# Kernel optimization log

Hardware: AMD Instinct MI355X
Metric: run time of the kernel (lower is better)

## Reference

```python
import jax, jax.numpy as jnp
import numpy as np

B, K, D = 8192, 256, 128


def setup_inputs() -> dict:
    key = jax.random.key(0)
    k1, k2 = jax.random.split(key)
    z = jax.random.normal(k1, (B, D), dtype=jnp.float32)
    centroids = jax.random.normal(k2, (K, D), dtype=jnp.float32)
    logvar = jnp.zeros((K, D), dtype=jnp.float32)
    return {"z": z, "centroids": centroids, "logvar": logvar}


def reference(z, centroids, logvar):
    # Mahalanobis (diagonal-covariance) distance of each z row to each centroid.
    # dist[b,k] = sum_d (z[b,d] - mu[k,d])^2 / var[k,d]
    diff = z[:, None, :] - centroids[None, :, :]          # (B, K, D)
    var = jnp.exp(logvar)[None, :, :]                      # (1, K, D)
    dist = jnp.sum(diff * diff / var, axis=2)              # (B, K)
    # Soft assignments: softmax over clusters of -0.5 * dist (stable softmax).
    return jax.nn.softmax(-0.5 * dist, axis=1)             # (B, K)
```

## Files before the change

### kernel.cpp

```cpp
#include <hip/hip_runtime.h>
#include <hip/hip_bf16.h>


typedef short     bf16x8  __attribute__((ext_vector_type(8)));
typedef float     f32x4   __attribute__((ext_vector_type(4)));
typedef unsigned short ushort_t;

constexpr int Bn = 8192, Kn = 256, Dn = 128;

constexpr size_t BH_OFF = 0;
constexpr size_t BL_OFF = (size_t)16 * 8 * 64 * 8;
constexpr size_t CV_OFF = 2 * BL_OFF;
constexpr size_t NEED_BYTES = CV_OFF * 2 + (size_t)Kn * 4;

__device__ __forceinline__ short bfbits(__hip_bfloat16 h) {
    return __builtin_bit_cast(short, h);
}

__device__ __forceinline__ void split8(const float* f, bf16x8& hi, bf16x8& lo) {
    #pragma unroll
    for (int p = 0; p < 4; ++p) {
        const float2 fp = make_float2(f[2 * p], f[2 * p + 1]);
        const __hip_bfloat162 h2 = __float22bfloat162_rn(fp);
        hi[2 * p]     = bfbits(h2.x);
        hi[2 * p + 1] = bfbits(h2.y);
        const float2 rp = make_float2(fp.x - __bfloat162float(h2.x),
                                      fp.y - __bfloat162float(h2.y));
        const __hip_bfloat162 l2 = __float22bfloat162_rn(rp);
        lo[2 * p]     = bfbits(l2.x);
        lo[2 * p + 1] = bfbits(l2.y);
    }
}

__global__ __launch_bounds__(512)
void prep(const float* __restrict__ cent, const float* __restrict__ lvar,
          ushort_t* __restrict__ ws)
{
    __shared__ float red2[16][8];
    const int tid = threadIdx.x;
    const int kk  = tid >> 6;
    const int l   = tid & 63;
    const int lg  = l >> 4;
    const int ll  = l & 15;
    const int cg  = blockIdx.x;
    const int col = cg * 16 + ll;
    const int d0  = kk * 16 + lg * 4;

    const float4 cv = *reinterpret_cast<const float4*>(cent + (size_t)col * Dn + d0);
    const float4 l4 = *reinterpret_cast<const float4*>(lvar + (size_t)col * Dn + d0);
    const float a0 = __expf(-l4.x), a1 = __expf(-l4.y);
    const float a2 = __expf(-l4.z), a3 = __expf(-l4.w);
    const float f[8] = {a0, -2.0f * cv.x * a0, a1, -2.0f * cv.y * a1,
                        a2, -2.0f * cv.z * a2, a3, -2.0f * cv.w * a3};
    bf16x8 hi, lo;
    split8(f, hi, lo);
    const size_t off = ((size_t)(cg * 8 + kk) * 64 + l) * 8;
    *reinterpret_cast<bf16x8*>(ws + BH_OFF + off) = hi;
    *reinterpret_cast<bf16x8*>(ws + BL_OFF + off) = lo;

    float cp = cv.x * cv.x * a0 + cv.y * cv.y * a1 +
               cv.z * cv.z * a2 + cv.w * cv.w * a3;
    cp += __shfl_xor(cp, 16);
    cp += __shfl_xor(cp, 32);
    if (lg == 0) red2[ll][kk] = cp;
    __syncthreads();
    if (tid < 16) {
        float s = 0.f;
        #pragma unroll
        for (int q = 0; q < 8; ++q) s += red2[tid][q];
        reinterpret_cast<float*>(ws + CV_OFF)[cg * 16 + tid] = s;
    }
}

__global__ __launch_bounds__(1024, 4)
void gmm_main(const float* __restrict__ z, const ushort_t* __restrict__ ws,
              float* __restrict__ out)
{
    __shared__ ushort_t Ah[2 * 8 * 64 * 8];
    __shared__ ushort_t Al[2 * 8 * 64 * 8];
    __shared__ float red[32][16];

    const int tid = threadIdx.x;
    const int w   = tid >> 6;
    const int l   = tid & 63;
    const int lg  = l >> 4;
    const int ll  = l & 15;
    const int b0  = blockIdx.x * 32;
    const int n0  = w * 16;

    {
        const int r   = tid >> 9;
        const int kks = (tid >> 6) & 7;
        const int row = r * 16 + ll;
        const int d0  = kks * 16 + lg * 4;
        const float4 v = *reinterpret_cast<const float4*>(
            z + (size_t)(b0 + row) * Dn + d0);
        const float f[8] = {v.x * v.x, v.x, v.y * v.y, v.y,
                            v.z * v.z, v.z, v.w * v.w, v.w};
        bf16x8 hi, lo;
        split8(f, hi, lo);
        const int off = tid * 8;
        *reinterpret_cast<bf16x8*>(&Ah[off]) = hi;
        *reinterpret_cast<bf16x8*>(&Al[off]) = lo;
    }
    __syncthreads();

    const ushort_t* BH = ws + BH_OFF;
    const ushort_t* BL = ws + BL_OFF;
    const float*  cvec = reinterpret_cast<const float*>(ws + CV_OFF);

    f32x4 acc0 = (f32x4){0.f, 0.f, 0.f, 0.f};
    f32x4 acc1 = (f32x4){0.f, 0.f, 0.f, 0.f};

    const size_t bbase = (size_t)w * 4096 + (size_t)l * 8;

    bf16x8 bh = *reinterpret_cast<const bf16x8*>(BH + bbase);
    bf16x8 bl = *reinterpret_cast<const bf16x8*>(BL + bbase);

    #pragma unroll
    for (int kk = 0; kk < 8; ++kk) {
        bf16x8 nbh, nbl;
        if (kk < 7) {
            nbh = *reinterpret_cast<const bf16x8*>(BH + bbase + (kk + 1) * 512);
            nbl = *reinterpret_cast<const bf16x8*>(BL + bbase + (kk + 1) * 512);
        }
        const int ao = kk * 512 + l * 8;
        const bf16x8 a0h = *reinterpret_cast<const bf16x8*>(&Ah[ao]);
        const bf16x8 a0l = *reinterpret_cast<const bf16x8*>(&Al[ao]);
        const bf16x8 a1h = *reinterpret_cast<const bf16x8*>(&Ah[4096 + ao]);
        const bf16x8 a1l = *reinterpret_cast<const bf16x8*>(&Al[4096 + ao]);

        acc0 = __builtin_amdgcn_mfma_f32_16x16x32_bf16(a0h, bh, acc0, 0, 0, 0);
        acc1 = __builtin_amdgcn_mfma_f32_16x16x32_bf16(a1h, bh, acc1, 0, 0, 0);
        acc0 = __builtin_amdgcn_mfma_f32_16x16x32_bf16(a0h, bl, acc0, 0, 0, 0);
        acc1 = __builtin_amdgcn_mfma_f32_16x16x32_bf16(a1h, bl, acc1, 0, 0, 0);
        acc0 = __builtin_amdgcn_mfma_f32_16x16x32_bf16(a0l, bh, acc0, 0, 0, 0);
        acc1 = __builtin_amdgcn_mfma_f32_16x16x32_bf16(a1l, bh, acc1, 0, 0, 0);

        bh = nbh; bl = nbl;
    }

    const float ck = cvec[n0 + ll];

    float dv[2][4];
    #pragma unroll
    for (int r = 0; r < 4; ++r) { dv[0][r] = acc0[r] + ck; dv[1][r] = acc1[r] + ck; }

    #pragma unroll
    for (int mi = 0; mi < 2; ++mi)
        #pragma unroll
        for (int r = 0; r < 4; ++r) {
            float t = dv[mi][r];
            t = fminf(t, __shfl_xor(t, 1));
            t = fminf(t, __shfl_xor(t, 2));
            t = fminf(t, __shfl_xor(t, 4));
            t = fminf(t, __shfl_xor(t, 8));
            if (ll == 0) red[mi * 16 + lg * 4 + r][w] = t;
        }
    __syncthreads();

    float gm[2][4];
    #pragma unroll
    for (int mi = 0; mi < 2; ++mi)
        #pragma unroll
        for (int r = 0; r < 4; ++r) {
            const int row = mi * 16 + lg * 4 + r;
            const f32x4* rp = reinterpret_cast<const f32x4*>(&red[row][0]);
            f32x4 m4 = rp[0];
            #pragma unroll
            for (int q = 1; q < 4; ++q) {
                f32x4 v = rp[q];
                m4[0] = fminf(m4[0], v[0]); m4[1] = fminf(m4[1], v[1]);
                m4[2] = fminf(m4[2], v[2]); m4[3] = fminf(m4[3], v[3]);
            }
            gm[mi][r] = fminf(fminf(m4[0], m4[1]), fminf(m4[2], m4[3]));
        }
    __syncthreads();

    float pv[2][4];
    #pragma unroll
    for (int mi = 0; mi < 2; ++mi)
        #pragma unroll
        for (int r = 0; r < 4; ++r) {
            const float p = __expf(-0.5f * (dv[mi][r] - gm[mi][r]));
            pv[mi][r] = p;
            float s = p;
            s += __shfl_xor(s, 1);
            s += __shfl_xor(s, 2);
            s += __shfl_xor(s, 4);
            s += __shfl_xor(s, 8);
            if (ll == 0) red[mi * 16 + lg * 4 + r][w] = s;
        }
    __syncthreads();

    #pragma unroll
    for (int mi = 0; mi < 2; ++mi)
        #pragma unroll
        for (int r = 0; r < 4; ++r) {
            const int row = mi * 16 + lg * 4 + r;
            const f32x4* rp = reinterpret_cast<const f32x4*>(&red[row][0]);
            f32x4 s4 = rp[0];
            #pragma unroll
            for (int q = 1; q < 4; ++q) {
                f32x4 v = rp[q];
                s4[0] += v[0]; s4[1] += v[1]; s4[2] += v[2]; s4[3] += v[3];
            }
            const float inv = 1.0f / ((s4[0] + s4[1]) + (s4[2] + s4[3]));
            out[(size_t)(b0 + row) * Kn + n0 + ll] = pv[mi][r] * inv;
        }
}

__global__ __launch_bounds__(1024, 4)
void gmm_fused(const float* __restrict__ z, const float* __restrict__ cent,
               const float* __restrict__ lvar, float* __restrict__ out)
{
    __shared__ ushort_t Ah[2 * 8 * 64 * 8];
    __shared__ ushort_t Al[2 * 8 * 64 * 8];
    __shared__ float red[32][16];

    const int tid = threadIdx.x;
    const int w   = tid >> 6;
    const int l   = tid & 63;
    const int lg  = l >> 4;
    const int ll  = l & 15;
    const int b0  = blockIdx.x * 32;
    const int n0  = w * 16;

    {
        const int r   = tid >> 9;
        const int kks = (tid >> 6) & 7;
        const int row = r * 16 + ll;
        const int d0  = kks * 16 + lg * 4;
        const float4 v = *reinterpret_cast<const float4*>(
            z + (size_t)(b0 + row) * Dn + d0);
        const float f[8] = {v.x * v.x, v.x, v.y * v.y, v.y,
                            v.z * v.z, v.z, v.w * v.w, v.w};
        bf16x8 hi, lo;
        split8(f, hi, lo);
        const int off = tid * 8;
        *reinterpret_cast<bf16x8*>(&Ah[off]) = hi;
        *reinterpret_cast<bf16x8*>(&Al[off]) = lo;
    }
    __syncthreads();

    f32x4 acc0 = (f32x4){0.f, 0.f, 0.f, 0.f};
    f32x4 acc1 = (f32x4){0.f, 0.f, 0.f, 0.f};
    float cpart = 0.0f;
    const size_t crow = (size_t)(n0 + ll) * Dn + lg * 4;

    float4 cv = *reinterpret_cast<const float4*>(cent + crow);
    float4 v4 = *reinterpret_cast<const float4*>(lvar + crow);

    #pragma unroll
    for (int kk = 0; kk < 8; ++kk) {
        float4 ncv, nv4;
        if (kk < 7) {
            ncv = *reinterpret_cast<const float4*>(cent + crow + (kk + 1) * 16);
            nv4 = *reinterpret_cast<const float4*>(lvar + crow + (kk + 1) * 16);
        }
        const float a0 = __expf(-v4.x), a1 = __expf(-v4.y);
        const float a2 = __expf(-v4.z), a3 = __expf(-v4.w);
        const float f[8] = {a0, -2.0f * cv.x * a0, a1, -2.0f * cv.y * a1,
                            a2, -2.0f * cv.z * a2, a3, -2.0f * cv.w * a3};
        bf16x8 Bh, Bl;
        split8(f, Bh, Bl);
        cpart += cv.x * cv.x * a0 + cv.y * cv.y * a1 +
                 cv.z * cv.z * a2 + cv.w * cv.w * a3;

        const int ao = kk * 512 + l * 8;
        const bf16x8 a0h = *reinterpret_cast<const bf16x8*>(&Ah[ao]);
        const bf16x8 a0l = *reinterpret_cast<const bf16x8*>(&Al[ao]);
        const bf16x8 a1h = *reinterpret_cast<const bf16x8*>(&Ah[4096 + ao]);
        const bf16x8 a1l = *reinterpret_cast<const bf16x8*>(&Al[4096 + ao]);

        acc0 = __builtin_amdgcn_mfma_f32_16x16x32_bf16(a0h, Bh, acc0, 0, 0, 0);
        acc1 = __builtin_amdgcn_mfma_f32_16x16x32_bf16(a1h, Bh, acc1, 0, 0, 0);
        acc0 = __builtin_amdgcn_mfma_f32_16x16x32_bf16(a0h, Bl, acc0, 0, 0, 0);
        acc1 = __builtin_amdgcn_mfma_f32_16x16x32_bf16(a1h, Bl, acc1, 0, 0, 0);
        acc0 = __builtin_amdgcn_mfma_f32_16x16x32_bf16(a0l, Bh, acc0, 0, 0, 0);
        acc1 = __builtin_amdgcn_mfma_f32_16x16x32_bf16(a1l, Bh, acc1, 0, 0, 0);

        cv = ncv; v4 = nv4;
    }
    cpart += __shfl_xor(cpart, 16);
    cpart += __shfl_xor(cpart, 32);
    const float ck = cpart;

    float dv[2][4];
    #pragma unroll
    for (int r = 0; r < 4; ++r) { dv[0][r] = acc0[r] + ck; dv[1][r] = acc1[r] + ck; }

    #pragma unroll
    for (int mi = 0; mi < 2; ++mi)
        #pragma unroll
        for (int r = 0; r < 4; ++r) {
            float t = dv[mi][r];
            t = fminf(t, __shfl_xor(t, 1));
            t = fminf(t, __shfl_xor(t, 2));
            t = fminf(t, __shfl_xor(t, 4));
            t = fminf(t, __shfl_xor(t, 8));
            if (ll == 0) red[mi * 16 + lg * 4 + r][w] = t;
        }
    __syncthreads();

    float gm[2][4];
    #pragma unroll
    for (int mi = 0; mi < 2; ++mi)
        #pragma unroll
        for (int r = 0; r < 4; ++r) {
            const int row = mi * 16 + lg * 4 + r;
            const f32x4* rp = reinterpret_cast<const f32x4*>(&red[row][0]);
            f32x4 m4 = rp[0];
            #pragma unroll
            for (int q = 1; q < 4; ++q) {
                f32x4 v = rp[q];
                m4[0] = fminf(m4[0], v[0]); m4[1] = fminf(m4[1], v[1]);
                m4[2] = fminf(m4[2], v[2]); m4[3] = fminf(m4[3], v[3]);
            }
            gm[mi][r] = fminf(fminf(m4[0], m4[1]), fminf(m4[2], m4[3]));
        }
    __syncthreads();

    float pv[2][4];
    #pragma unroll
    for (int mi = 0; mi < 2; ++mi)
        #pragma unroll
        for (int r = 0; r < 4; ++r) {
            const float p = __expf(-0.5f * (dv[mi][r] - gm[mi][r]));
            pv[mi][r] = p;
            float s = p;
            s += __shfl_xor(s, 1);
            s += __shfl_xor(s, 2);
            s += __shfl_xor(s, 4);
            s += __shfl_xor(s, 8);
            if (ll == 0) red[mi * 16 + lg * 4 + r][w] = s;
        }
    __syncthreads();

    #pragma unroll
    for (int mi = 0; mi < 2; ++mi)
        #pragma unroll
        for (int r = 0; r < 4; ++r) {
            const int row = mi * 16 + lg * 4 + r;
            const f32x4* rp = reinterpret_cast<const f32x4*>(&red[row][0]);
            f32x4 s4 = rp[0];
            #pragma unroll
            for (int q = 1; q < 4; ++q) {
                f32x4 v = rp[q];
                s4[0] += v[0]; s4[1] += v[1]; s4[2] += v[2]; s4[3] += v[3];
            }
            const float inv = 1.0f / ((s4[0] + s4[1]) + (s4[2] + s4[3]));
            out[(size_t)(b0 + row) * Kn + n0 + ll] = pv[mi][r] * inv;
        }
}

extern "C" void kernel_launch(void* const* d_in, const int* in_sizes, int n_in,
                              void* d_out, int out_size, void* d_ws, size_t ws_size,
                              hipStream_t stream) {
    const float* z      = (const float*)d_in[0];
    const float* cent   = (const float*)d_in[1];
    const float* logvar = (const float*)d_in[2];
    float* out = (float*)d_out;
    (void)in_sizes; (void)n_in; (void)out_size;

    if (ws_size >= NEED_BYTES) {
        ushort_t* ws = (ushort_t*)d_ws;
        hipLaunchKernelGGL(prep, dim3(16), dim3(512), 0, stream,
                           cent, logvar, ws);
        hipLaunchKernelGGL(gmm_main, dim3(Bn / 32), dim3(1024), 0, stream,
                           z, (const ushort_t*)ws, out);
    } else {
        hipLaunchKernelGGL(gmm_fused, dim3(Bn / 32), dim3(1024), 0, stream,
                           z, cent, logvar, out);
    }
}
```

Before: 22.57 us.

## Halve rows per block in gmm_main to double grid size and occupancy

gmm_main now handles 16 batch rows per block instead of 32, launching 512 blocks, each wave keeping one accumulator instead of two. Launch bounds are raised to allow 8 blocks per CU. The cross-wave max and sum reductions now happen in wave 0 and are broadcast through shared memory. The aim is more parallelism and better latency hiding on the short GEMM-plus-softmax. The cost is that every block reloads the full centroid B operand from the workspace for half as many rows, and the explicit register prefetch of B is dropped.

Measured after the change: 20.87 us. 7.5% less time.

```diff
diff --git a/kernel.cpp b/kernel.cpp
--- a/kernel.cpp
+++ b/kernel.cpp
@@ -72,9 +72,116 @@
     }
 }
 
-__global__ __launch_bounds__(1024, 4)
+__global__ __launch_bounds__(1024, 8)
 void gmm_main(const float* __restrict__ z, const ushort_t* __restrict__ ws,
               float* __restrict__ out)
+{
+    __shared__ ushort_t Ah[8 * 64 * 8];
+    __shared__ ushort_t Al[8 * 64 * 8];
+    __shared__ float red[16][16];
+    __shared__ float gsc[2][16];
+
+    const int tid = threadIdx.x;
+    const int w   = tid >> 6;
+    const int l   = tid & 63;
+    const int lg  = l >> 4;
+    const int ll  = l & 15;
+    const int b0  = blockIdx.x * 16;
+    const int n0  = w * 16;
+
+    if (tid < 512) {
+        const int kks = tid >> 6;
+        const int d0  = kks * 16 + lg * 4;
+        const float4 v = *reinterpret_cast<const float4*>(
+            z + (size_t)(b0 + ll) * Dn + d0);
+        const float f[8] = {v.x * v.x, v.x, v.y * v.y, v.y,
+                            v.z * v.z, v.z, v.w * v.w, v.w};
+        bf16x8 hi, lo;
+        split8(f, hi, lo);
+        const int off = tid * 8;
+        *reinterpret_cast<bf16x8*>(&Ah[off]) = hi;
+        *reinterpret_cast<bf16x8*>(&Al[off]) = lo;
+    }
+    __syncthreads();
+
+    const ushort_t* BH = ws + BH_OFF;
+    const ushort_t* BL = ws + BL_OFF;
+    const float*  cvec = reinterpret_cast<const float*>(ws + CV_OFF);
+
+    f32x4 acc = (f32x4){0.f, 0.f, 0.f, 0.f};
+    const size_t bbase = ((size_t)w * 8 * 64 + l) * 8;
+
+    #pragma unroll
+    for (int kk = 0; kk < 8; ++kk) {
+        const bf16x8 bh = *reinterpret_cast<const bf16x8*>(BH + bbase + kk * 512);
+        const bf16x8 bl = *reinterpret_cast<const bf16x8*>(BL + bbase + kk * 512);
+        const int ao = kk * 512 + l * 8;
+        const bf16x8 ah = *reinterpret_cast<const bf16x8*>(&Ah[ao]);
+        const bf16x8 al = *reinterpret_cast<const bf16x8*>(&Al[ao]);
+
+        acc = __builtin_amdgcn_mfma_f32_16x16x32_bf16(ah, bh, acc, 0, 0, 0);
+        acc = __builtin_amdgcn_mfma_f32_16x16x32_bf16(ah, bl, acc, 0, 0, 0);
+        acc = __builtin_amdgcn_mfma_f32_16x16x32_bf16(al, bh, acc, 0, 0, 0);
+    }
+
+    const float ck = cvec[n0 + ll];
+    float dv[4], pv[4];
+    #pragma unroll
+    for (int r = 0; r < 4; ++r) dv[r] = acc[r] + ck;
+
+    #pragma unroll
+    for (int r = 0; r < 4; ++r) {
+        float t = dv[r];
+        t = fminf(t, __shfl_xor(t, 1));
+        t = fminf(t, __shfl_xor(t, 2));
+        t = fminf(t, __shfl_xor(t, 4));
+        t = fminf(t, __shfl_xor(t, 8));
+        if (ll == 0) red[lg * 4 + r][w] = t;
+    }
+    __syncthreads();
+
+    if (w == 0) {
+        const int row = l >> 2, q = l & 3;
+        const f32x4 v = *reinterpret_cast<const f32x4*>(&red[row][q * 4]);
+        float m = fminf(fminf(v[0], v[1]), fminf(v[2], v[3]));
+        m = fminf(m, __shfl_xor(m, 1));
+        m = fminf(m, __shfl_xor(m, 2));
+        if (q == 0) gsc[0][row] = m;
+    }
+    __syncthreads();
+
+    #pragma unroll
+    for (int r = 0; r < 4; ++r) {
+        pv[r] = __expf(-0.5f * (dv[r] - gsc[0][lg * 4 + r]));
+        float s = pv[r];
+        s += __shfl_xor(s, 1);
+        s += __shfl_xor(s, 2);
+        s += __shfl_xor(s, 4);
+        s += __shfl_xor(s, 8);
+        if (ll == 0) red[lg * 4 + r][w] = s;
+    }
+    __syncthreads();
+
+    if (w == 0) {
+        const int row = l >> 2, q = l & 3;
+        const f32x4 v = *reinterpret_cast<const f32x4*>(&red[row][q * 4]);
+        float s = (v[0] + v[1]) + (v[2] + v[3]);
+        s += __shfl_xor(s, 1);
+        s += __shfl_xor(s, 2);
+        if (q == 0) gsc[1][row] = 1.0f / s;
+    }
+    __syncthreads();
+
+    #pragma unroll
+    for (int r = 0; r < 4; ++r) {
+        const int row = lg * 4 + r;
+        out[(size_t)(b0 + row) * Kn + n0 + ll] = pv[r] * gsc[1][row];
+    }
+}
+
+__global__ __launch_bounds__(1024, 4)
+void gmm_fused(const float* __restrict__ z, const float* __restrict__ cent,
+               const float* __restrict__ lvar, float* __restrict__ out)
 {
     __shared__ ushort_t Ah[2 * 8 * 64 * 8];
     __shared__ ushort_t Al[2 * 8 * 64 * 8];
@@ -105,42 +212,48 @@
     }
     __syncthreads();
 
-    const ushort_t* BH = ws + BH_OFF;
-    const ushort_t* BL = ws + BL_OFF;
-    const float*  cvec = reinterpret_cast<const float*>(ws + CV_OFF);
-
     f32x4 acc0 = (f32x4){0.f, 0.f, 0.f, 0.f};
     f32x4 acc1 = (f32x4){0.f, 0.f, 0.f, 0.f};
-
-    const size_t bbase = (size_t)w * 4096 + (size_t)l * 8;
-
-    bf16x8 bh = *reinterpret_cast<const bf16x8*>(BH + bbase);
-    bf16x8 bl = *reinterpret_cast<const bf16x8*>(BL + bbase);
+    float cpart = 0.0f;
+    const size_t crow = (size_t)(n0 + ll) * Dn + lg * 4;
+
+    float4 cv = *reinterpret_cast<const float4*>(cent + crow);
+    float4 v4 = *reinterpret_cast<const float4*>(lvar + crow);
 
     #pragma unroll
     for (int kk = 0; kk < 8; ++kk) {
-        bf16x8 nbh, nbl;
+        float4 ncv, nv4;
         if (kk < 7) {
-            nbh = *reinterpret_cast<const bf16x8*>(BH + bbase + (kk + 1) * 512);
-            nbl = *reinterpret_cast<const bf16x8*>(BL + bbase + (kk + 1) * 512);
-        }
+            ncv = *reinterpret_cast<const float4*>(cent + crow + (kk + 1) * 16);
+            nv4 = *reinterpret_cast<const float4*>(lvar + crow + (kk + 1) * 16);
+        }
+        const float a0 = __expf(-v4.x), a1 = __expf(-v4.y);
+        const float a2 = __expf(-v4.z), a3 = __expf(-v4.w);
+        const float f[8] = {a0, -2.0f * cv.x * a0, a1, -2.0f * cv.y * a1,
+                            a2, -2.0f * cv.z * a2, a3, -2.0f * cv.w * a3};
+        bf16x8 Bh, Bl;
+        split8(f, Bh, Bl);
+        cpart += cv.x * cv.x * a0 + cv.y * cv.y * a1 +
+                 cv.z * cv.z * a2 + cv.w * cv.w * a3;
+
         const int ao = kk * 512 + l * 8;
         const bf16x8 a0h = *reinterpret_cast<const bf16x8*>(&Ah[ao]);
         const bf16x8 a0l = *reinterpret_cast<const bf16x8*>(&Al[ao]);
         const bf16x8 a1h = *reinterpret_cast<const bf16x8*>(&Ah[4096 + ao]);
         const bf16x8 a1l = *reinterpret_cast<const bf16x8*>(&Al[4096 + ao]);
 
-        acc0 = __builtin_amdgcn_mfma_f32_16x16x32_bf16(a0h, bh, acc0, 0, 0, 0);
-        acc1 = __builtin_amdgcn_mfma_f32_16x16x32_bf16(a1h, bh, acc1, 0, 0, 0);
-        acc0 = __builtin_amdgcn_mfma_f32_16x16x32_bf16(a0h, bl, acc0, 0, 0, 0);
-        acc1 = __builtin_amdgcn_mfma_f32_16x16x32_bf16(a1h, bl, acc1, 0, 0, 0);
-        acc0 = __builtin_amdgcn_mfma_f32_16x16x32_bf16(a0l, bh, acc0, 0, 0, 0);
-        acc1 = __builtin_amdgcn_mfma_f32_16x16x32_bf16(a1l, bh, acc1, 0, 0, 0);
-
-        bh = nbh; bl = nbl;
-    }
-
-    const float ck = cvec[n0 + ll];
+        acc0 = __builtin_amdgcn_mfma_f32_16x16x32_bf16(a0h, Bh, acc0, 0, 0, 0);
+        acc1 = __builtin_amdgcn_mfma_f32_16x16x32_bf16(a1h, Bh, acc1, 0, 0, 0);
+        acc0 = __builtin_amdgcn_mfma_f32_16x16x32_bf16(a0h, Bl, acc0, 0, 0, 0);
+        acc1 = __builtin_amdgcn_mfma_f32_16x16x32_bf16(a1h, Bl, acc1, 0, 0, 0);
+        acc0 = __builtin_amdgcn_mfma_f32_16x16x32_bf16(a0l, Bh, acc0, 0, 0, 0);
+        acc1 = __builtin_amdgcn_mfma_f32_16x16x32_bf16(a1l, Bh, acc1, 0, 0, 0);
+
+        cv = ncv; v4 = nv4;
+    }
+    cpart += __shfl_xor(cpart, 16);
+    cpart += __shfl_xor(cpart, 32);
+    const float ck = cpart;
 
     float dv[2][4];
     #pragma unroll
@@ -210,150 +323,6 @@
         }
 }
 
-__global__ __launch_bounds__(1024, 4)
-void gmm_fused(const float* __restrict__ z, const float* __restrict__ cent,
-               const float* __restrict__ lvar, float* __restrict__ out)
-{
-    __shared__ ushort_t Ah[2 * 8 * 64 * 8];
-    __shared__ ushort_t Al[2 * 8 * 64 * 8];
-    __shared__ float red[32][16];
-
-    const int tid = threadIdx.x;
-    const int w   = tid >> 6;
-    const int l   = tid & 63;
-    const int lg  = l >> 4;
-    const int ll  = l & 15;
-    const int b0  = blockIdx.x * 32;
-    const int n0  = w * 16;
-
-    {
-        const int r   = tid >> 9;
-        const int kks = (tid >> 6) & 7;
-        const int row = r * 16 + ll;
-        const int d0  = kks * 16 + lg * 4;
-        const float4 v = *reinterpret_cast<const float4*>(
-            z + (size_t)(b0 + row) * Dn + d0);
-        const float f[8] = {v.x * v.x, v.x, v.y * v.y, v.y,
-                            v.z * v.z, v.z, v.w * v.w, v.w};
-        bf16x8 hi, lo;
-        split8(f, hi, lo);
-        const int off = tid * 8;
-        *reinterpret_cast<bf16x8*>(&Ah[off]) = hi;
-        *reinterpret_cast<bf16x8*>(&Al[off]) = lo;
-    }
-    __syncthreads();
-
-    f32x4 acc0 = (f32x4){0.f, 0.f, 0.f, 0.f};
-    f32x4 acc1 = (f32x4){0.f, 0.f, 0.f, 0.f};
-    float cpart = 0.0f;
-    const size_t crow = (size_t)(n0 + ll) * Dn + lg * 4;
-
-    float4 cv = *reinterpret_cast<const float4*>(cent + crow);
-    float4 v4 = *reinterpret_cast<const float4*>(lvar + crow);
-
-    #pragma unroll
-    for (int kk = 0; kk < 8; ++kk) {
-        float4 ncv, nv4;
-        if (kk < 7) {
-            ncv = *reinterpret_cast<const float4*>(cent + crow + (kk + 1) * 16);
-            nv4 = *reinterpret_cast<const float4*>(lvar + crow + (kk + 1) * 16);
-        }
-        const float a0 = __expf(-v4.x), a1 = __expf(-v4.y);
-        const float a2 = __expf(-v4.z), a3 = __expf(-v4.w);
-        const float f[8] = {a0, -2.0f * cv.x * a0, a1, -2.0f * cv.y * a1,
-                            a2, -2.0f * cv.z * a2, a3, -2.0f * cv.w * a3};
-        bf16x8 Bh, Bl;
-        split8(f, Bh, Bl);
-        cpart += cv.x * cv.x * a0 + cv.y * cv.y * a1 +
-                 cv.z * cv.z * a2 + cv.w * cv.w * a3;
-
-        const int ao = kk * 512 + l * 8;
-        const bf16x8 a0h = *reinterpret_cast<const bf16x8*>(&Ah[ao]);
-        const bf16x8 a0l = *reinterpret_cast<const bf16x8*>(&Al[ao]);
-        const bf16x8 a1h = *reinterpret_cast<const bf16x8*>(&Ah[4096 + ao]);
-        const bf16x8 a1l = *reinterpret_cast<const bf16x8*>(&Al[4096 + ao]);
-
-        acc0 = __builtin_amdgcn_mfma_f32_16x16x32_bf16(a0h, Bh, acc0, 0, 0, 0);
-        acc1 = __builtin_amdgcn_mfma_f32_16x16x32_bf16(a1h, Bh, acc1, 0, 0, 0);
-        acc0 = __builtin_amdgcn_mfma_f32_16x16x32_bf16(a0h, Bl, acc0, 0, 0, 0);
-        acc1 = __builtin_amdgcn_mfma_f32_16x16x32_bf16(a1h, Bl, acc1, 0, 0, 0);
-        acc0 = __builtin_amdgcn_mfma_f32_16x16x32_bf16(a0l, Bh, acc0, 0, 0, 0);
-        acc1 = __builtin_amdgcn_mfma_f32_16x16x32_bf16(a1l, Bh, acc1, 0, 0, 0);
-
-        cv = ncv; v4 = nv4;
-    }
-    cpart += __shfl_xor(cpart, 16);
-    cpart += __shfl_xor(cpart, 32);
-    const float ck = cpart;
-
-    float dv[2][4];
-    #pragma unroll
-    for (int r = 0; r < 4; ++r) { dv[0][r] = acc0[r] + ck; dv[1][r] = acc1[r] + ck; }
-
-    #pragma unroll
-    for (int mi = 0; mi < 2; ++mi)
-        #pragma unroll
-        for (int r = 0; r < 4; ++r) {
-            float t = dv[mi][r];
-            t = fminf(t, __shfl_xor(t, 1));
-            t = fminf(t, __shfl_xor(t, 2));
-            t = fminf(t, __shfl_xor(t, 4));
-            t = fminf(t, __shfl_xor(t, 8));
-            if (ll == 0) red[mi * 16 + lg * 4 + r][w] = t;
-        }
-    __syncthreads();
-
-    float gm[2][4];
-    #pragma unroll
-    for (int mi = 0; mi < 2; ++mi)
-        #pragma unroll
-        for (int r = 0; r < 4; ++r) {
-            const int row = mi * 16 + lg * 4 + r;
-            const f32x4* rp = reinterpret_cast<const f32x4*>(&red[row][0]);
-            f32x4 m4 = rp[0];
-            #pragma unroll
-            for (int q = 1; q < 4; ++q) {
-                f32x4 v = rp[q];
-                m4[0] = fminf(m4[0], v[0]); m4[1] = fminf(m4[1], v[1]);
-                m4[2] = fminf(m4[2], v[2]); m4[3] = fminf(m4[3], v[3]);
-            }
-            gm[mi][r] = fminf(fminf(m4[0], m4[1]), fminf(m4[2], m4[3]));
-        }
-    __syncthreads();
-
-    float pv[2][4];
-    #pragma unroll
-    for (int mi = 0; mi < 2; ++mi)
-        #pragma unroll
-        for (int r = 0; r < 4; ++r) {
-            const float p = __expf(-0.5f * (dv[mi][r] - gm[mi][r]));
-            pv[mi][r] = p;
-            float s = p;
-            s += __shfl_xor(s, 1);
-            s += __shfl_xor(s, 2);
-            s += __shfl_xor(s, 4);
-            s += __shfl_xor(s, 8);
-            if (ll == 0) red[mi * 16 + lg * 4 + r][w] = s;
-        }
-    __syncthreads();
-
-    #pragma unroll
-    for (int mi = 0; mi < 2; ++mi)
-        #pragma unroll
-        for (int r = 0; r < 4; ++r) {
-            const int row = mi * 16 + lg * 4 + r;
-            const f32x4* rp = reinterpret_cast<const f32x4*>(&red[row][0]);
-            f32x4 s4 = rp[0];
-            #pragma unroll
-            for (int q = 1; q < 4; ++q) {
-                f32x4 v = rp[q];
-                s4[0] += v[0]; s4[1] += v[1]; s4[2] += v[2]; s4[3] += v[3];
-            }
-            const float inv = 1.0f / ((s4[0] + s4[1]) + (s4[2] + s4[3]));
-            out[(size_t)(b0 + row) * Kn + n0 + ll] = pv[mi][r] * inv;
-        }
-}
-
 extern "C" void kernel_launch(void* const* d_in, const int* in_sizes, int n_in,
                               void* d_out, int out_size, void* d_ws, size_t ws_size,
                               hipStream_t stream) {
@@ -367,7 +336,7 @@
         ushort_t* ws = (ushort_t*)d_ws;
         hipLaunchKernelGGL(prep, dim3(16), dim3(512), 0, stream,
                            cent, logvar, ws);
-        hipLaunchKernelGGL(gmm_main, dim3(Bn / 32), dim3(1024), 0, stream,
+        hipLaunchKernelGGL(gmm_main, dim3(Bn / 16), dim3(1024), 0, stream,
                            z, (const ushort_t*)ws, out);
     } else {
         hipLaunchKernelGGL(gmm_fused, dim3(Bn / 32), dim3(1024), 0, stream,
```
